# Kernel optimization log

Hardware: AMD Instinct MI355X
Metric: run time of the kernel (lower is better)

Reference implementation:

```python
import jax, jax.numpy as jnp
import numpy as np

B, N, F_DIM, E, C = 8, 16384, 64, 262144, 10
BN_EPS = 1e-5


def setup_inputs() -> dict:
    key = jax.random.key(0)
    ks = jax.random.split(key, 10)
    s = 1.0 / np.sqrt(F_DIM)
    return {
        "x": jax.random.normal(ks[0], (B, N, F_DIM), jnp.float32),
        "edge_src": jax.random.randint(ks[1], (B, E), 0, N, jnp.int32),
        "edge_dst": jax.random.randint(ks[2], (B, E), 0, N, jnp.int32),
        "W1": jax.random.normal(ks[3], (F_DIM, F_DIM), jnp.float32) * s,
        "b1": jax.random.normal(ks[4], (F_DIM,), jnp.float32) * 0.01,
        "W2": jax.random.normal(ks[5], (F_DIM, F_DIM), jnp.float32) * s,
        "b2": jax.random.normal(ks[6], (F_DIM,), jnp.float32) * 0.01,
        "bn_gamma": jnp.ones((F_DIM,), jnp.float32),
        "bn_beta": jnp.zeros((F_DIM,), jnp.float32),
        "lin_W": jax.random.normal(ks[7], (C, N * F_DIM), jnp.float32) * (1.0 / np.sqrt(N * F_DIM)),
        "lin_b": jax.random.normal(ks[8], (C,), jnp.float32) * 0.01,
    }


def _graph_conv(x, src, dst, W, b):
    # DGL GraphConv, norm='both', in_feats == out_feats (aggregate-first path):
    # h = D_in^{-1/2} * A * (D_out^{-1/2} * x) @ W + b, degrees clamped to >= 1.
    ones = jnp.ones((src.shape[0],), x.dtype)
    deg_out = jnp.maximum(jax.ops.segment_sum(ones, src, num_segments=N), 1.0)
    deg_in = jnp.maximum(jax.ops.segment_sum(ones, dst, num_segments=N), 1.0)
    xs = x * jax.lax.rsqrt(deg_out)[:, None]          # [N, F]
    agg = jax.ops.segment_sum(xs[src], dst, num_segments=N)  # gather + scatter-add
    rst = agg * jax.lax.rsqrt(deg_in)[:, None]
    return rst @ W + b


def reference(x, edge_src, edge_dst, W1, b1, W2, b2, bn_gamma, bn_beta, lin_W, lin_b):
    conv = jax.vmap(_graph_conv, in_axes=(0, 0, 0, None, None))
    h = jax.nn.relu(conv(x, edge_src, edge_dst, W1, b1))  # conv1 + relu
    # dropout p=0.0 (eval): identity
    h = conv(h, edge_src, edge_dst, W2, b2)               # conv2 -> [B, N, F]
    # BatchNorm1d over channel F (torch normalizes over B and N in training mode)
    mean = jnp.mean(h, axis=(0, 1))
    var = jnp.var(h, axis=(0, 1))
    h = bn_gamma * (h - mean) * jax.lax.rsqrt(var + BN_EPS) + bn_beta
    flat = h.reshape(B, N * F_DIM)
    return flat @ lin_W.T + lin_b                         # [B, C]
```

## Files before the change

### kernel.cpp

```cpp
#include <hip/hip_runtime.h>

#define B_     8
#define N_     16384
#define F_     64
#define E_     262144
#define C_     10
#define NF_    (N_ * F_)
#define BN_    (B_ * N_)
#define BNF_   (B_ * N_ * F_)
#define BE_    (B_ * E_)
#define CAP_   48
#define CHUNK_ 4096
#define NCH_   (E_ / CHUNK_)
#define NW_    (N_ / 4)
#define NSB_   4096
#define NFB_   1024
#define EPS_   1e-5f

typedef _Float16 h8 __attribute__((ext_vector_type(8)));
typedef _Float16 h4 __attribute__((ext_vector_type(4)));
typedef float f32x4 __attribute__((ext_vector_type(4)));

#define SWZ(r, o) ((((r) * 64 + (o))) ^ (((r) & 7) << 3))

__global__ __launch_bounds__(256) void k_count(const int* __restrict__ src,
                                               const int* __restrict__ dst,
                                               unsigned int* __restrict__ partO,
                                               unsigned int* __restrict__ partI,
                                               const float* __restrict__ W1,
                                               const float* __restrict__ W2,
                                               _Float16* __restrict__ Wt1,
                                               _Float16* __restrict__ Wt2) {
    __shared__ unsigned int pO[NW_];
    __shared__ unsigned int pI[NW_];
    int t = threadIdx.x;
    if (blockIdx.x >= B_ * NCH_) {
        int g = blockIdx.x - B_ * NCH_;
        const float* Ws = (g & 8) ? W2 : W1;
        _Float16* Wd = (g & 8) ? Wt2 : Wt1;
        int c0 = (g & 7) * 512;
        for (int j = t; j < 512; j += 256) {
            int o = c0 + j;
            Wd[o] = (_Float16)Ws[(o & 63) * 64 + (o >> 6)];
        }
        return;
    }
    int b = blockIdx.x & 7, c = blockIdx.x >> 3;
    for (int i = t; i < NW_; i += 256) { pO[i] = 0; pI[i] = 0; }
    __syncthreads();
    const int* sb = src + (size_t)b * E_ + (size_t)c * CHUNK_;
    const int* db = dst + (size_t)b * E_ + (size_t)c * CHUNK_;
    for (int i = t; i < CHUNK_; i += 256) {
        int s = sb[i], d = db[i];
        atomicAdd(&pO[s >> 2], 1u << ((s & 3) * 8));
        atomicAdd(&pI[d >> 2], 1u << ((d & 3) * 8));
    }
    __syncthreads();
    size_t base = (size_t)(b * NCH_ + c) * NW_;
    for (int i = t; i < NW_; i += 256) {
        partO[base + i] = pO[i];
        partI[base + i] = pI[i];
    }
}

__global__ __launch_bounds__(256) void k_offsets(const unsigned int* __restrict__ partO,
                                                 const unsigned int* __restrict__ partI,
                                                 unsigned int* __restrict__ baseArr,
                                                 float* __restrict__ degOr,
                                                 float* __restrict__ degIr,
                                                 int* __restrict__ cntI_g) {
    int gw = blockIdx.x * 256 + threadIdx.x;
    int b = gw >> 12;
    int rw = gw & 4095;
    unsigned int sumI = 0, sumO = 0;
    for (int c = 0; c < NCH_; ++c) {
        size_t idx = (size_t)(b * NCH_ + c) * NW_ + rw;
        unsigned int wI = partI[idx];
        baseArr[idx] = sumI;
        sumI += wI;
        sumO += partO[idx];
    }
    int row0 = gw * 4;
#pragma unroll
    for (int r = 0; r < 4; ++r) {
        unsigned int ci = (sumI >> (r * 8)) & 0xFFu;
        unsigned int co = (sumO >> (r * 8)) & 0xFFu;
        degIr[row0 + r] = rsqrtf(fmaxf((float)ci, 1.0f));
        degOr[row0 + r] = rsqrtf(fmaxf((float)co, 1.0f));
        cntI_g[row0 + r] = (int)ci;
    }
}

__global__ __launch_bounds__(256) void k_fill(const int* __restrict__ src,
                                              const int* __restrict__ dst,
                                              const unsigned int* __restrict__ baseArr,
                                              unsigned short* __restrict__ csr) {
    __shared__ unsigned int cur[NW_];
    __shared__ unsigned int bw[NW_];
    int t = threadIdx.x;
    int b = blockIdx.x & 7, c = blockIdx.x >> 3;
    size_t pbase = (size_t)(b * NCH_ + c) * NW_;
    for (int i = t; i < NW_; i += 256) { cur[i] = 0; bw[i] = baseArr[pbase + i]; }
    __syncthreads();
    const int* sb = src + (size_t)b * E_ + (size_t)c * CHUNK_;
    const int* db = dst + (size_t)b * E_ + (size_t)c * CHUNK_;
    unsigned short* cb = csr + (size_t)b * N_ * CAP_;
    for (int i = t; i < CHUNK_; i += 256) {
        int s = sb[i], d = db[i];
        unsigned int sh = (d & 3) * 8;
        unsigned int old = atomicAdd(&cur[d >> 2], 1u << sh);
        unsigned int pos = ((old >> sh) & 0xFFu) + ((bw[d >> 2] >> sh) & 0xFFu);
        if (pos < CAP_) cb[d * CAP_ + pos] = (unsigned short)s;
    }
}

template <bool IN16, bool SCALE>
__global__ __launch_bounds__(256) void k_mmf(const float* __restrict__ in32,
                                             const _Float16* __restrict__ in16,
                                             const _Float16* __restrict__ Wt,
                                             const float* __restrict__ rs,
                                             _Float16* __restrict__ out) {
    __shared__ _Float16 Al[4096];
    __shared__ _Float16 Bl[4096];
    int t = threadIdx.x;
    int bat = blockIdx.x & 7;
    int rowg = bat * N_ + (blockIdx.x >> 3) * 64;

#pragma unroll
    for (int j = 0; j < 2; ++j) {
        int c = t + j * 256;
        int r = c >> 3, o = (c & 7) * 8;
        *(h8*)&Al[SWZ(r, o)] = *(const h8*)(Wt + c * 8);
    }
#pragma unroll
    for (int j = 0; j < 2; ++j) {
        int c = t + j * 256;
        int r = c >> 3, o = (c & 7) * 8;
        h8 v;
        if constexpr (IN16) {
            v = *(const h8*)(in16 + (size_t)(rowg + r) * 64 + o);
        } else {
            const float4* p = (const float4*)(in32 + (size_t)(rowg + r) * 64 + o);
            float4 x0 = p[0], x1 = p[1];
            v[0] = (_Float16)x0.x; v[1] = (_Float16)x0.y;
            v[2] = (_Float16)x0.z; v[3] = (_Float16)x0.w;
            v[4] = (_Float16)x1.x; v[5] = (_Float16)x1.y;
            v[6] = (_Float16)x1.z; v[7] = (_Float16)x1.w;
        }
        *(h8*)&Bl[SWZ(r, o)] = v;
    }
    __syncthreads();

    int lane = t & 63;
    int w = t >> 6;
    int lm = lane & 15;
    int lk = (lane >> 4) * 8;
    f32x4 acc0 = {0.f, 0.f, 0.f, 0.f}, acc1 = {0.f, 0.f, 0.f, 0.f};
    f32x4 acc2 = {0.f, 0.f, 0.f, 0.f}, acc3 = {0.f, 0.f, 0.f, 0.f};
#pragma unroll
    for (int ks = 0; ks < 2; ++ks) {
        h8 a = *(const h8*)&Al[SWZ(w * 16 + lm, lk + ks * 32)];
        h8 vb0 = *(const h8*)&Bl[SWZ(0 + lm, lk + ks * 32)];
        h8 vb1 = *(const h8*)&Bl[SWZ(16 + lm, lk + ks * 32)];
        h8 vb2 = *(const h8*)&Bl[SWZ(32 + lm, lk + ks * 32)];
        h8 vb3 = *(const h8*)&Bl[SWZ(48 + lm, lk + ks * 32)];
        acc0 = __builtin_amdgcn_mfma_f32_16x16x32_f16(a, vb0, acc0, 0, 0, 0);
        acc1 = __builtin_amdgcn_mfma_f32_16x16x32_f16(a, vb1, acc1, 0, 0, 0);
        acc2 = __builtin_amdgcn_mfma_f32_16x16x32_f16(a, vb2, acc2, 0, 0, 0);
        acc3 = __builtin_amdgcn_mfma_f32_16x16x32_f16(a, vb3, acc3, 0, 0, 0);
    }
    int fo = w * 16 + (lane >> 4) * 4;
#define STORE_TILE(ACC, RT)                                                    \
    {                                                                          \
        int row = rowg + (RT) * 16 + lm;                                       \
        float scv = SCALE ? rs[row] : 1.0f;                                    \
        h4 ov;                                                                 \
        ov[0] = (_Float16)(ACC[0] * scv); ov[1] = (_Float16)(ACC[1] * scv);    \
        ov[2] = (_Float16)(ACC[2] * scv); ov[3] = (_Float16)(ACC[3] * scv);    \
        *(h4*)(out + (size_t)row * 64 + fo) = ov;                              \
    }
    STORE_TILE(acc0, 0)
    STORE_TILE(acc1, 1)
    STORE_TILE(acc2, 2)
    STORE_TILE(acc3, 3)
#undef STORE_TILE
}

template <bool CONV1>
__global__ __launch_bounds__(256, 6) void k_gat(
        const int* __restrict__ cnt, const unsigned short* __restrict__ csr,
        const _Float16* __restrict__ z, const float* __restrict__ degIr,
        const float* __restrict__ degOr, const float* __restrict__ bias,
        _Float16* __restrict__ out16, float* __restrict__ pstat) {
    __shared__ float sS[4][64];
    __shared__ float sQ[4][64];
    int t = threadIdx.x;
    int lane = t & 63;
    int wave = t >> 6;
    int c8 = lane & 7;
    int b = blockIdx.x & 7;
    int row = (blockIdx.x >> 3) * 32 + wave * 8 + (lane >> 3);
    int wid = b * N_ + row;
    const _Float16* zb = z + (size_t)b * NF_;
    int lb = lane & 56;
    int ho = c8 * 8;

    int n = cnt[wid];
    if (n > CAP_) n = CAP_;
    size_t cb = (size_t)wid * CAP_;
    int e0 = csr[cb + c8] & 0x3FFF;
    int e1 = csr[cb + 8 + c8] & 0x3FFF;
    int e2 = csr[cb + 16 + c8] & 0x3FFF;
    int e3 = csr[cb + 24 + c8] & 0x3FFF;
    int e4 = csr[cb + 32 + c8] & 0x3FFF;
    int e5 = csr[cb + 40 + c8] & 0x3FFF;
    float dIr = degIr[wid];
    float4 bv0 = *(const float4*)(bias + ho);
    float4 bv1 = *(const float4*)(bias + ho + 4);
    int m = n;
    m = max(m, __shfl_xor(m, 8));
    m = max(m, __shfl_xor(m, 16));
    m = max(m, __shfl_xor(m, 32));

    float af[8];
#pragma unroll
    for (int i = 0; i < 8; ++i) af[i] = 0.0f;

#define SEG(EREG, KOFF)                                                        \
    {                                                                          \
        int rem = n - (KOFF);                                                  \
        h8 v[8];                                                               \
        _Pragma("unroll")                                                      \
        for (int jj = 0; jj < 8; ++jj) {                                       \
            int s = __shfl(EREG, lb + jj);                                     \
            h8 vv = {};                                                        \
            if (jj < rem) vv = *(const h8*)(zb + s * 64 + ho);                 \
            v[jj] = vv;                                                        \
        }                                                                      \
        h8 s0 = v[0] + v[1], s1 = v[2] + v[3];                                 \
        h8 s2 = v[4] + v[5], s3 = v[6] + v[7];                                 \
        h8 s4 = s0 + s1, s5 = s2 + s3;                                         \
        h8 s6 = s4 + s5;                                                       \
        _Pragma("unroll")                                                      \
        for (int i = 0; i < 8; ++i) af[i] += (float)s6[i];                     \
    }

    SEG(e0, 0)
    if (m > 8)  SEG(e1, 8)
    if (m > 16) SEG(e2, 16)
    if (m > 24) SEG(e3, 24)
    if (m > 32) SEG(e4, 32)
    if (m > 40) SEG(e5, 40)
#undef SEG

    float bb[8] = {bv0.x, bv0.y, bv0.z, bv0.w, bv1.x, bv1.y, bv1.z, bv1.w};
    if constexpr (CONV1) {
        float po = degOr[wid];
        h8 ov;
#pragma unroll
        for (int i = 0; i < 8; ++i) {
            ov[i] = (_Float16)(fmaxf(fmaf(af[i], dIr, bb[i]), 0.0f) * po);
        }
        *(h8*)(out16 + (size_t)wid * 64 + ho) = ov;
    } else {
        float vv[8];
        h8 ov;
#pragma unroll
        for (int i = 0; i < 8; ++i) {
            vv[i] = fmaf(af[i], dIr, bb[i]);
            ov[i] = (_Float16)vv[i];
        }
        *(h8*)(out16 + (size_t)wid * 64 + ho) = ov;
        float ssv[8], qqv[8];
#pragma unroll
        for (int i = 0; i < 8; ++i) { ssv[i] = vv[i]; qqv[i] = vv[i] * vv[i]; }
#pragma unroll
        for (int i = 0; i < 8; ++i) {
            ssv[i] += __shfl_xor(ssv[i], 8);  qqv[i] += __shfl_xor(qqv[i], 8);
            ssv[i] += __shfl_xor(ssv[i], 16); qqv[i] += __shfl_xor(qqv[i], 16);
            ssv[i] += __shfl_xor(ssv[i], 32); qqv[i] += __shfl_xor(qqv[i], 32);
        }
        if (lane < 8) {
#pragma unroll
            for (int i = 0; i < 8; ++i) {
                sS[wave][lane * 8 + i] = ssv[i];
                sQ[wave][lane * 8 + i] = qqv[i];
            }
        }
        __syncthreads();
        if (t < 64) {
            float s_ = sS[0][t] + sS[1][t] + sS[2][t] + sS[3][t];
            float q_ = sQ[0][t] + sQ[1][t] + sQ[2][t] + sQ[3][t];
            pstat[(size_t)blockIdx.x * 128 + t] = s_;
            pstat[(size_t)blockIdx.x * 128 + 64 + t] = q_;
        }
    }
}

__global__ __launch_bounds__(256) void k_red(const float* __restrict__ part,
                                             float* __restrict__ stats2) {
    __shared__ float sred[256];
    int t = threadIdx.x;
    int half = t >> 7;
    int s = t & 127;
    int r0 = blockIdx.x * (NSB_ / 32);
    float acc = 0.0f;
    for (int k = 0; k < NSB_ / 32 / 2; ++k) {
        acc += part[(size_t)(r0 + k * 2 + half) * 128 + s];
    }
    sred[t] = acc;
    __syncthreads();
    if (t < 128) stats2[blockIdx.x * 128 + t] = sred[t] + sred[t + 128];
}

__global__ void k_bnfin(const float* __restrict__ stats2, const float* __restrict__ gamma,
                        const float* __restrict__ beta, float* __restrict__ sc,
                        float* __restrict__ sh) {
    int f = threadIdx.x;
    if (f < 64) {
        float sum = 0.0f, sq = 0.0f;
        for (int j = 0; j < 32; ++j) {
            sum += stats2[j * 128 + f];
            sq  += stats2[j * 128 + 64 + f];
        }
        float inv = 1.0f / (float)BN_;
        float mean = sum * inv;
        float var  = sq * inv - mean * mean;
        float s = gamma[f] * rsqrtf(var + EPS_);
        sc[f] = s;
        sh[f] = beta[f] - mean * s;
    }
}

__global__ __launch_bounds__(256) void k_final(
        const _Float16* __restrict__ h, const float* __restrict__ linW,
        const float* __restrict__ sc, const float* __restrict__ sh,
        float* __restrict__ pf) {
    int t = threadIdx.x;
    int lane = t & 63;
    int wv = t >> 6;
    int b0 = wv * 2, b1 = wv * 2 + 1;
    int base = blockIdx.x * (NF_ / NFB_);
    float s = sc[lane], shv = sh[lane];
    float acc[C_][2];
#pragma unroll
    for (int c = 0; c < C_; ++c) { acc[c][0] = 0.0f; acc[c][1] = 0.0f; }

#pragma unroll 4
    for (int k = 0; k < 16; ++k) {
        int i = base + k * 64 + lane;
        float h0 = fmaf((float)h[(size_t)b0 * NF_ + i], s, shv);
        float h1 = fmaf((float)h[(size_t)b1 * NF_ + i], s, shv);
#pragma unroll
        for (int c = 0; c < C_; ++c) {
            float w = linW[(size_t)c * NF_ + i];
            acc[c][0] = fmaf(h0, w, acc[c][0]);
            acc[c][1] = fmaf(h1, w, acc[c][1]);
        }
    }

#pragma unroll
    for (int c = 0; c < C_; ++c) {
#pragma unroll
        for (int j = 0; j < 2; ++j) {
            float v = acc[c][j];
            v += __shfl_down(v, 32);
            v += __shfl_down(v, 16);
            v += __shfl_down(v, 8);
            v += __shfl_down(v, 4);
            v += __shfl_down(v, 2);
            v += __shfl_down(v, 1);
            acc[c][j] = v;
        }
    }
    if (lane == 0) {
        float* p = pf + (size_t)blockIdx.x * 80;
#pragma unroll
        for (int c = 0; c < C_; ++c) {
            p[b0 * C_ + c] = acc[c][0];
            p[b1 * C_ + c] = acc[c][1];
        }
    }
}

__global__ __launch_bounds__(64) void k_fsum(const float* __restrict__ pf,
                                             const float* __restrict__ linb,
                                             float* __restrict__ out) {
    int o = blockIdx.x;
    int lane = threadIdx.x;
    float acc = 0.0f;
#pragma unroll
    for (int k = 0; k < 16; ++k) {
        acc += pf[(size_t)(k * 64 + lane) * 80 + o];
    }
    acc += __shfl_down(acc, 32);
    acc += __shfl_down(acc, 16);
    acc += __shfl_down(acc, 8);
    acc += __shfl_down(acc, 4);
    acc += __shfl_down(acc, 2);
    acc += __shfl_down(acc, 1);
    if (lane == 0) out[o] = acc + linb[o % C_];
}

extern "C" void kernel_launch(void* const* d_in, const int* in_sizes, int n_in,
                              void* d_out, int out_size, void* d_ws, size_t ws_size,
                              hipStream_t stream) {
    const float* x        = (const float*)d_in[0];
    const int*   edge_src = (const int*)d_in[1];
    const int*   edge_dst = (const int*)d_in[2];
    const float* W1       = (const float*)d_in[3];
    const float* b1       = (const float*)d_in[4];
    const float* W2       = (const float*)d_in[5];
    const float* b2       = (const float*)d_in[6];
    const float* gamma    = (const float*)d_in[7];
    const float* beta     = (const float*)d_in[8];
    const float* linW     = (const float*)d_in[9];
    const float* linb     = (const float*)d_in[10];
    float* out = (float*)d_out;

    char* w = (char*)d_ws;
    float* degOr = (float*)w;           w += BN_ * 4;
    float* degIr = (float*)w;           w += BN_ * 4;
    int*   cntI  = (int*)w;             w += BN_ * 4;
    unsigned short* csr = (unsigned short*)w; w += (size_t)BN_ * CAP_ * 2;
    _Float16* z    = (_Float16*)w;      w += (size_t)BNF_ * 2;
    _Float16* h1z  = (_Float16*)w;      w += (size_t)BNF_ * 2;
    _Float16* h2h  = (_Float16*)w;      w += (size_t)BNF_ * 2;
    unsigned int* partO   = (unsigned int*)w;  w += (size_t)B_ * NCH_ * NW_ * 4;
    unsigned int* partI   = (unsigned int*)w;  w += (size_t)B_ * NCH_ * NW_ * 4;
    unsigned int* baseArr = (unsigned int*)w;  w += (size_t)B_ * NCH_ * NW_ * 4;
    float* partStats = (float*)w;       w += (size_t)NSB_ * 128 * 4;
    float* stats2 = (float*)w;          w += 32 * 128 * 4;
    float* pf    = (float*)w;           w += (size_t)NFB_ * 80 * 4;
    float* sc    = (float*)w;           w += 64 * 4;
    float* sh    = (float*)w;           w += 64 * 4;
    _Float16* Wt1 = (_Float16*)w;       w += 4096 * 2;
    _Float16* Wt2 = (_Float16*)w;       w += 4096 * 2;

    k_count<<<B_ * NCH_ + 16, 256, 0, stream>>>(edge_src, edge_dst, partO, partI,
                                                W1, W2, Wt1, Wt2);
    k_offsets<<<BN_ / 4 / 256, 256, 0, stream>>>(partO, partI, baseArr, degOr, degIr, cntI);
    k_fill<<<B_ * NCH_, 256, 0, stream>>>(edge_src, edge_dst, baseArr, csr);

    k_mmf<false, true><<<BN_ / 64, 256, 0, stream>>>(x, nullptr, Wt1, degOr, z);
    k_gat<true><<<BN_ / 32, 256, 0, stream>>>(cntI, csr, z, degIr, degOr, b1, h1z, nullptr);

    k_mmf<true, false><<<BN_ / 64, 256, 0, stream>>>(nullptr, h1z, Wt2, nullptr, z);
    k_gat<false><<<BN_ / 32, 256, 0, stream>>>(cntI, csr, z, degIr, nullptr, b2, h2h, partStats);

    k_red<<<32, 256, 0, stream>>>(partStats, stats2);
    k_bnfin<<<1, 64, 0, stream>>>(stats2, gamma, beta, sc, sh);
    k_final<<<NFB_, 256, 0, stream>>>(h2h, linW, sc, sh, pf);
    k_fsum<<<80, 64, 0, stream>>>(pf, linb, out);
}
```

Measured before the change: 239.2 us.

## Build CSR with global atomics in one pass and fuse BN finalize into final GEMV

Replaces the three-kernel count/prefix/fill CSR build, which used per-chunk packed 8-bit shared histograms, with a single kernel that uses global atomicAdd on per-node counters to claim slots directly, after a memset. Degree rsqrt is now computed on the fly from integer counts in the consumers instead of being stored. The BN finalize kernel is folded into k_final, and k_final is vectorized to load h4/float4. This cuts launches and intermediate passes over the edge lists, but relies on global atomic throughput and makes CSR slot order nondeterministic, which changes summation order.

```diff
diff --git a/kernel.cpp b/kernel.cpp
--- a/kernel.cpp
+++ b/kernel.cpp
@@ -10,9 +10,6 @@
 #define BNF_   (B_ * N_ * F_)
 #define BE_    (B_ * E_)
 #define CAP_   48
-#define CHUNK_ 4096
-#define NCH_   (E_ / CHUNK_)
-#define NW_    (N_ / 4)
 #define NSB_   4096
 #define NFB_   1024
 #define EPS_   1e-5f
@@ -23,19 +20,18 @@
 
 #define SWZ(r, o) ((((r) * 64 + (o))) ^ (((r) & 7) << 3))
 
-__global__ __launch_bounds__(256) void k_count(const int* __restrict__ src,
+__global__ __launch_bounds__(256) void k_build(const int* __restrict__ src,
                                                const int* __restrict__ dst,
-                                               unsigned int* __restrict__ partO,
-                                               unsigned int* __restrict__ partI,
+                                               int* __restrict__ cntI,
+                                               int* __restrict__ cntO,
+                                               unsigned short* __restrict__ csr,
                                                const float* __restrict__ W1,
                                                const float* __restrict__ W2,
                                                _Float16* __restrict__ Wt1,
                                                _Float16* __restrict__ Wt2) {
-    __shared__ unsigned int pO[NW_];
-    __shared__ unsigned int pI[NW_];
     int t = threadIdx.x;
-    if (blockIdx.x >= B_ * NCH_) {
-        int g = blockIdx.x - B_ * NCH_;
+    if (blockIdx.x >= B_ * 256) {
+        int g = blockIdx.x - B_ * 256;
         const float* Ws = (g & 8) ? W2 : W1;
         _Float16* Wd = (g & 8) ? Wt2 : Wt1;
         int c0 = (g & 7) * 512;
@@ -46,71 +42,20 @@
         return;
     }
     int b = blockIdx.x & 7, c = blockIdx.x >> 3;
-    for (int i = t; i < NW_; i += 256) { pO[i] = 0; pI[i] = 0; }
-    __syncthreads();
-    const int* sb = src + (size_t)b * E_ + (size_t)c * CHUNK_;
-    const int* db = dst + (size_t)b * E_ + (size_t)c * CHUNK_;
-    for (int i = t; i < CHUNK_; i += 256) {
-        int s = sb[i], d = db[i];
-        atomicAdd(&pO[s >> 2], 1u << ((s & 3) * 8));
-        atomicAdd(&pI[d >> 2], 1u << ((d & 3) * 8));
-    }
-    __syncthreads();
-    size_t base = (size_t)(b * NCH_ + c) * NW_;
-    for (int i = t; i < NW_; i += 256) {
-        partO[base + i] = pO[i];
-        partI[base + i] = pI[i];
-    }
-}
-
-__global__ __launch_bounds__(256) void k_offsets(const unsigned int* __restrict__ partO,
-                                                 const unsigned int* __restrict__ partI,
-                                                 unsigned int* __restrict__ baseArr,
-                                                 float* __restrict__ degOr,
-                                                 float* __restrict__ degIr,
-                                                 int* __restrict__ cntI_g) {
-    int gw = blockIdx.x * 256 + threadIdx.x;
-    int b = gw >> 12;
-    int rw = gw & 4095;
-    unsigned int sumI = 0, sumO = 0;
-    for (int c = 0; c < NCH_; ++c) {
-        size_t idx = (size_t)(b * NCH_ + c) * NW_ + rw;
-        unsigned int wI = partI[idx];
-        baseArr[idx] = sumI;
-        sumI += wI;
-        sumO += partO[idx];
-    }
-    int row0 = gw * 4;
-#pragma unroll
-    for (int r = 0; r < 4; ++r) {
-        unsigned int ci = (sumI >> (r * 8)) & 0xFFu;
-        unsigned int co = (sumO >> (r * 8)) & 0xFFu;
-        degIr[row0 + r] = rsqrtf(fmaxf((float)ci, 1.0f));
-        degOr[row0 + r] = rsqrtf(fmaxf((float)co, 1.0f));
-        cntI_g[row0 + r] = (int)ci;
-    }
-}
-
-__global__ __launch_bounds__(256) void k_fill(const int* __restrict__ src,
-                                              const int* __restrict__ dst,
-                                              const unsigned int* __restrict__ baseArr,
-                                              unsigned short* __restrict__ csr) {
-    __shared__ unsigned int cur[NW_];
-    __shared__ unsigned int bw[NW_];
-    int t = threadIdx.x;
-    int b = blockIdx.x & 7, c = blockIdx.x >> 3;
-    size_t pbase = (size_t)(b * NCH_ + c) * NW_;
-    for (int i = t; i < NW_; i += 256) { cur[i] = 0; bw[i] = baseArr[pbase + i]; }
-    __syncthreads();
-    const int* sb = src + (size_t)b * E_ + (size_t)c * CHUNK_;
-    const int* db = dst + (size_t)b * E_ + (size_t)c * CHUNK_;
+    const int4* sb = (const int4*)(src + (size_t)b * E_ + (size_t)c * 1024);
+    const int4* db = (const int4*)(dst + (size_t)b * E_ + (size_t)c * 1024);
+    int* cI = cntI + b * N_;
+    int* cO = cntO + b * N_;
     unsigned short* cb = csr + (size_t)b * N_ * CAP_;
-    for (int i = t; i < CHUNK_; i += 256) {
-        int s = sb[i], d = db[i];
-        unsigned int sh = (d & 3) * 8;
-        unsigned int old = atomicAdd(&cur[d >> 2], 1u << sh);
-        unsigned int pos = ((old >> sh) & 0xFFu) + ((bw[d >> 2] >> sh) & 0xFFu);
-        if (pos < CAP_) cb[d * CAP_ + pos] = (unsigned short)s;
+    int4 s4 = sb[t];
+    int4 d4 = db[t];
+#pragma unroll
+    for (int j = 0; j < 4; ++j) {
+        int s = ((const int*)&s4)[j];
+        int d = ((const int*)&d4)[j];
+        atomicAdd(cO + s, 1);
+        int pos = atomicAdd(cI + d, 1);
+        if (pos < CAP_) cb[(size_t)d * CAP_ + pos] = (unsigned short)s;
     }
 }
 
@@ -118,7 +63,7 @@
 __global__ __launch_bounds__(256) void k_mmf(const float* __restrict__ in32,
                                              const _Float16* __restrict__ in16,
                                              const _Float16* __restrict__ Wt,
-                                             const float* __restrict__ rs,
+                                             const int* __restrict__ cntO,
                                              _Float16* __restrict__ out) {
     __shared__ _Float16 Al[4096];
     __shared__ _Float16 Bl[4096];
@@ -173,7 +118,7 @@
 #define STORE_TILE(ACC, RT)                                                    \
     {                                                                          \
         int row = rowg + (RT) * 16 + lm;                                       \
-        float scv = SCALE ? rs[row] : 1.0f;                                    \
+        float scv = SCALE ? rsqrtf(fmaxf((float)cntO[row], 1.0f)) : 1.0f;      \
         h4 ov;                                                                 \
         ov[0] = (_Float16)(ACC[0] * scv); ov[1] = (_Float16)(ACC[1] * scv);    \
         ov[2] = (_Float16)(ACC[2] * scv); ov[3] = (_Float16)(ACC[3] * scv);    \
@@ -188,10 +133,10 @@
 
 template <bool CONV1>
 __global__ __launch_bounds__(256, 6) void k_gat(
-        const int* __restrict__ cnt, const unsigned short* __restrict__ csr,
-        const _Float16* __restrict__ z, const float* __restrict__ degIr,
-        const float* __restrict__ degOr, const float* __restrict__ bias,
-        _Float16* __restrict__ out16, float* __restrict__ pstat) {
+        const int* __restrict__ cnt, const int* __restrict__ cntO,
+        const unsigned short* __restrict__ csr, const _Float16* __restrict__ z,
+        const float* __restrict__ bias, _Float16* __restrict__ out16,
+        float* __restrict__ pstat) {
     __shared__ float sS[4][64];
     __shared__ float sQ[4][64];
     int t = threadIdx.x;
@@ -206,6 +151,7 @@
     int ho = c8 * 8;
 
     int n = cnt[wid];
+    float dIr = rsqrtf(fmaxf((float)n, 1.0f));
     if (n > CAP_) n = CAP_;
     size_t cb = (size_t)wid * CAP_;
     int e0 = csr[cb + c8] & 0x3FFF;
@@ -214,7 +160,6 @@
     int e3 = csr[cb + 24 + c8] & 0x3FFF;
     int e4 = csr[cb + 32 + c8] & 0x3FFF;
     int e5 = csr[cb + 40 + c8] & 0x3FFF;
-    float dIr = degIr[wid];
     float4 bv0 = *(const float4*)(bias + ho);
     float4 bv1 = *(const float4*)(bias + ho + 4);
     int m = n;
@@ -255,7 +200,7 @@
 
     float bb[8] = {bv0.x, bv0.y, bv0.z, bv0.w, bv1.x, bv1.y, bv1.z, bv1.w};
     if constexpr (CONV1) {
-        float po = degOr[wid];
+        float po = rsqrtf(fmaxf((float)cntO[wid], 1.0f));
         h8 ov;
 #pragma unroll
         for (int i = 0; i < 8; ++i) {
@@ -313,49 +258,61 @@
     if (t < 128) stats2[blockIdx.x * 128 + t] = sred[t] + sred[t + 128];
 }
 
-__global__ void k_bnfin(const float* __restrict__ stats2, const float* __restrict__ gamma,
-                        const float* __restrict__ beta, float* __restrict__ sc,
-                        float* __restrict__ sh) {
-    int f = threadIdx.x;
-    if (f < 64) {
+__global__ __launch_bounds__(256) void k_final(
+        const _Float16* __restrict__ h, const float* __restrict__ linW,
+        const float* __restrict__ stats2, const float* __restrict__ gamma,
+        const float* __restrict__ beta, float* __restrict__ pf) {
+    __shared__ float scs[64], shs[64];
+    int t = threadIdx.x;
+    if (t < 64) {
         float sum = 0.0f, sq = 0.0f;
+#pragma unroll
         for (int j = 0; j < 32; ++j) {
-            sum += stats2[j * 128 + f];
-            sq  += stats2[j * 128 + 64 + f];
+            sum += stats2[j * 128 + t];
+            sq  += stats2[j * 128 + 64 + t];
         }
         float inv = 1.0f / (float)BN_;
         float mean = sum * inv;
         float var  = sq * inv - mean * mean;
-        float s = gamma[f] * rsqrtf(var + EPS_);
-        sc[f] = s;
-        sh[f] = beta[f] - mean * s;
-    }
-}
-
-__global__ __launch_bounds__(256) void k_final(
-        const _Float16* __restrict__ h, const float* __restrict__ linW,
-        const float* __restrict__ sc, const float* __restrict__ sh,
-        float* __restrict__ pf) {
-    int t = threadIdx.x;
+        float s = gamma[t] * rsqrtf(var + EPS_);
+        scs[t] = s;
+        shs[t] = beta[t] - mean * s;
+    }
+    __syncthreads();
+
     int lane = t & 63;
     int wv = t >> 6;
     int b0 = wv * 2, b1 = wv * 2 + 1;
     int base = blockIdx.x * (NF_ / NFB_);
-    float s = sc[lane], shv = sh[lane];
+    float4 s4  = *(const float4*)&scs[(lane & 15) * 4];
+    float4 sh4 = *(const float4*)&shs[(lane & 15) * 4];
     float acc[C_][2];
 #pragma unroll
     for (int c = 0; c < C_; ++c) { acc[c][0] = 0.0f; acc[c][1] = 0.0f; }
 
-#pragma unroll 4
-    for (int k = 0; k < 16; ++k) {
-        int i = base + k * 64 + lane;
-        float h0 = fmaf((float)h[(size_t)b0 * NF_ + i], s, shv);
-        float h1 = fmaf((float)h[(size_t)b1 * NF_ + i], s, shv);
+#pragma unroll
+    for (int k = 0; k < 4; ++k) {
+        int i = base + k * 256 + lane * 4;
+        h4 ha = *(const h4*)(h + (size_t)b0 * NF_ + i);
+        h4 hb = *(const h4*)(h + (size_t)b1 * NF_ + i);
+        float h0[4], h1[4];
+        h0[0] = fmaf((float)ha[0], s4.x, sh4.x);
+        h0[1] = fmaf((float)ha[1], s4.y, sh4.y);
+        h0[2] = fmaf((float)ha[2], s4.z, sh4.z);
+        h0[3] = fmaf((float)ha[3], s4.w, sh4.w);
+        h1[0] = fmaf((float)hb[0], s4.x, sh4.x);
+        h1[1] = fmaf((float)hb[1], s4.y, sh4.y);
+        h1[2] = fmaf((float)hb[2], s4.z, sh4.z);
+        h1[3] = fmaf((float)hb[3], s4.w, sh4.w);
 #pragma unroll
         for (int c = 0; c < C_; ++c) {
-            float w = linW[(size_t)c * NF_ + i];
-            acc[c][0] = fmaf(h0, w, acc[c][0]);
-            acc[c][1] = fmaf(h1, w, acc[c][1]);
+            float4 w4 = *(const float4*)(linW + (size_t)c * NF_ + i);
+            float a0 = acc[c][0], a1 = acc[c][1];
+            a0 = fmaf(h0[0], w4.x, a0); a0 = fmaf(h0[1], w4.y, a0);
+            a0 = fmaf(h0[2], w4.z, a0); a0 = fmaf(h0[3], w4.w, a0);
+            a1 = fmaf(h1[0], w4.x, a1); a1 = fmaf(h1[1], w4.y, a1);
+            a1 = fmaf(h1[2], w4.z, a1); a1 = fmaf(h1[3], w4.w, a1);
+            acc[c][0] = a0; acc[c][1] = a1;
         }
     }
 
@@ -419,37 +376,29 @@
     float* out = (float*)d_out;
 
     char* w = (char*)d_ws;
-    float* degOr = (float*)w;           w += BN_ * 4;
-    float* degIr = (float*)w;           w += BN_ * 4;
     int*   cntI  = (int*)w;             w += BN_ * 4;
+    int*   cntO  = (int*)w;             w += BN_ * 4;
     unsigned short* csr = (unsigned short*)w; w += (size_t)BN_ * CAP_ * 2;
     _Float16* z    = (_Float16*)w;      w += (size_t)BNF_ * 2;
     _Float16* h1z  = (_Float16*)w;      w += (size_t)BNF_ * 2;
     _Float16* h2h  = (_Float16*)w;      w += (size_t)BNF_ * 2;
-    unsigned int* partO   = (unsigned int*)w;  w += (size_t)B_ * NCH_ * NW_ * 4;
-    unsigned int* partI   = (unsigned int*)w;  w += (size_t)B_ * NCH_ * NW_ * 4;
-    unsigned int* baseArr = (unsigned int*)w;  w += (size_t)B_ * NCH_ * NW_ * 4;
     float* partStats = (float*)w;       w += (size_t)NSB_ * 128 * 4;
     float* stats2 = (float*)w;          w += 32 * 128 * 4;
     float* pf    = (float*)w;           w += (size_t)NFB_ * 80 * 4;
-    float* sc    = (float*)w;           w += 64 * 4;
-    float* sh    = (float*)w;           w += 64 * 4;
     _Float16* Wt1 = (_Float16*)w;       w += 4096 * 2;
     _Float16* Wt2 = (_Float16*)w;       w += 4096 * 2;
 
-    k_count<<<B_ * NCH_ + 16, 256, 0, stream>>>(edge_src, edge_dst, partO, partI,
-                                                W1, W2, Wt1, Wt2);
-    k_offsets<<<BN_ / 4 / 256, 256, 0, stream>>>(partO, partI, baseArr, degOr, degIr, cntI);
-    k_fill<<<B_ * NCH_, 256, 0, stream>>>(edge_src, edge_dst, baseArr, csr);
-
-    k_mmf<false, true><<<BN_ / 64, 256, 0, stream>>>(x, nullptr, Wt1, degOr, z);
-    k_gat<true><<<BN_ / 32, 256, 0, stream>>>(cntI, csr, z, degIr, degOr, b1, h1z, nullptr);
+    hipMemsetAsync(cntI, 0, (size_t)BN_ * 2 * sizeof(int), stream);
+    k_build<<<B_ * 256 + 16, 256, 0, stream>>>(edge_src, edge_dst, cntI, cntO,
+                                               csr, W1, W2, Wt1, Wt2);
+
+    k_mmf<false, true><<<BN_ / 64, 256, 0, stream>>>(x, nullptr, Wt1, cntO, z);
+    k_gat<true><<<BN_ / 32, 256, 0, stream>>>(cntI, cntO, csr, z, b1, h1z, nullptr);
 
     k_mmf<true, false><<<BN_ / 64, 256, 0, stream>>>(nullptr, h1z, Wt2, nullptr, z);
-    k_gat<false><<<BN_ / 32, 256, 0, stream>>>(cntI, csr, z, degIr, nullptr, b2, h2h, partStats);
+    k_gat<false><<<BN_ / 32, 256, 0, stream>>>(cntI, nullptr, csr, z, b2, h2h, partStats);
 
     k_red<<<32, 256, 0, stream>>>(partStats, stats2);
-    k_bnfin<<<1, 64, 0, stream>>>(stats2, gamma, beta, sc, sh);
-    k_final<<<NFB_, 256, 0, stream>>>(h2h, linW, sc, sh, pf);
+    k_final<<<NFB_, 256, 0, stream>>>(h2h, linW, stats2, gamma, beta, pf);
     k_fsum<<<80, 64, 0, stream>>>(pf, linb, out);
 }
```

New measurement: 380.4 us. 1.59x slower.
